# Performance work log

Hardware: AMD Instinct MI355X
Metric: run time of the kernel (lower is better)

## Reference

```python
import jax, jax.numpy as jnp
import numpy as np

N = 4096
IN_F = 128
OUT_F = 64      # per-head out_features
HEADS = 4
ALPHA = 0.2     # LeakyReLU negative slope
NEG_FILL = -9e15


def setup_inputs() -> dict:
    key = jax.random.key(0)
    k_h, k_adj, k_W, k_a = jax.random.split(key, 4)
    h = jax.random.normal(k_h, (N, IN_F), dtype=jnp.float32)
    adj = jax.random.randint(k_adj, (N, N), 0, 2, dtype=jnp.int32)
    W = jax.random.normal(k_W, (IN_F, OUT_F * HEADS), dtype=jnp.float32) * 0.1
    a = jax.random.normal(k_a, (2 * OUT_F, 1), dtype=jnp.float32) * 0.1
    bias = jnp.zeros((OUT_F * HEADS,), dtype=jnp.float32)
    return {"h": h, "adj": adj, "W": W, "a": a, "bias": bias}


def reference(h, adj, W, a, bias):
    n = h.shape[0]
    Wh = (h @ W).reshape(n, HEADS, OUT_F)            # (N, H, F)
    # e_ij = leakyrelu(a_left . Wh_i + a_right . Wh_j)  (decomposed outer sum;
    # same math as concat([Wh_i, Wh_j]) @ a in the original)
    a_left = a[:OUT_F, 0]                            # (F,)
    a_right = a[OUT_F:, 0]                           # (F,)
    left = jnp.einsum('nhf,f->nh', Wh, a_left)       # (N, H)
    right = jnp.einsum('nhf,f->nh', Wh, a_right)     # (N, H)
    mask = adj > 0                                   # (N, N)
    outs = []
    for head in range(HEADS):                        # small fixed loop over heads
        e = left[:, head, None] + right[None, :, head]          # (N, N)
        e = jnp.where(e >= 0, e, ALPHA * e)                      # LeakyReLU
        e = jnp.where(mask, e, NEG_FILL)
        attn = jax.nn.softmax(e, axis=1)                         # (N, N)
        outs.append(attn @ Wh[:, head, :])                       # (N, F)
    out = jnp.concatenate(outs, axis=1)              # concat=True -> (N, H*F)
    return out + bias
```

## Files before the change

kernel.cpp:

```cpp
#include <hip/hip_runtime.h>
#include <hip/hip_bf16.h>

#define NN 4096
#define IN_F 128
#define OUT_F 64
#define C_TOT 256
#define ALPHA 0.2f
#define LOG2E 1.4426950408889634f

typedef float f32x4 __attribute__((ext_vector_type(4)));
typedef __bf16 bf16x8 __attribute__((ext_vector_type(8)));

__device__ __forceinline__ unsigned fmap(float f) {
    unsigned u = __float_as_uint(f);
    return (u >> 31) ? ~u : (u | 0x80000000u);
}
__device__ __forceinline__ float funmap(unsigned u) {
    return (u >> 31) ? __uint_as_float(u & 0x7FFFFFFFu) : __uint_as_float(~u);
}
__device__ __forceinline__ unsigned short bfbits(float x) {
    union { __bf16 b; unsigned short u; } t;
    t.b = (__bf16)x;
    return t.u;
}
__device__ __forceinline__ void gl16(const void* g, void* l) {
    __builtin_amdgcn_global_load_lds((const __attribute__((address_space(1))) void*)g,
                                     (__attribute__((address_space(3))) void*)l, 16, 0, 0);
}
__device__ __forceinline__ void gl4(const void* g, void* l) {
    __builtin_amdgcn_global_load_lds((const __attribute__((address_space(1))) void*)g,
                                     (__attribute__((address_space(3))) void*)l, 4, 0, 0);
}

__global__ __launch_bounds__(256) void k_mask(
    const int* __restrict__ adj, unsigned* __restrict__ mask2,
    const float* __restrict__ W, const float* __restrict__ a,
    unsigned short* __restrict__ WTbf, float* __restrict__ uLR,
    unsigned int* __restrict__ Rmax)
{
    const int tid = threadIdx.x;
    const int lane = tid & 63, wv = tid >> 6;
    const int row = blockIdx.x * 4 + wv;
    const int* __restrict__ ar = adj + (size_t)row * NN;
    const int rg = row >> 6, r64 = row & 63;
    for (int c = 0; c < 8; ++c) {
        const int j0 = c * 512;
        unsigned w = 0u;
#pragma unroll
        for (int k = 0; k < 8; ++k) {
            const unsigned long long bb = __ballot(ar[j0 + k * 64 + lane] > 0);
            const unsigned lo = (unsigned)bb, hi = (unsigned)(bb >> 32);
            if ((lane >> 1) == k) w = (lane & 1) ? hi : lo;
        }
        if (lane < 16) {
            const int wi = c * 16 + lane;
            const int jq = wi >> 5, t = (wi >> 2) & 7, j4 = wi & 3;
            mask2[(size_t)(((rg * 4 + jq) * 8) + t) * 256 + r64 * 4 + j4] = w;
        }
    }

    if (blockIdx.x < 32) {
        const int b = blockIdx.x;
        const int c = b * 8 + (tid & 7);
#pragma unroll
        for (int pass = 0; pass < 4; ++pass) {
            const int k = pass * 32 + (tid >> 3);
            WTbf[(size_t)c * IN_F + k] = bfbits(W[k * C_TOT + c]);
        }
        if (b == 0) {
            if (tid < 4) Rmax[tid] = 0u;
            for (int o = tid; o < 1024; o += 256) {
                const int k = o >> 3, j = o & 7;
                const int hd = j & 3, side = j >> 2;
                float s = 0.f;
                for (int f = 0; f < OUT_F; ++f)
                    s = fmaf(W[k * C_TOT + hd * OUT_F + f], a[side * OUT_F + f], s);
                uLR[k * 8 + side * 4 + hd] = s;
            }
        }
    }
}

__global__ __launch_bounds__(256) void k_prep(
    const float* __restrict__ hmat, const unsigned short* __restrict__ WTbf,
    const float* __restrict__ uLR, unsigned short* __restrict__ WhT,
    float* __restrict__ leftT, float2* __restrict__ erPair,
    unsigned int* __restrict__ Rmax)
{
    __shared__ float hs[16][132];
    __shared__ float us[128][8];
    const int tid = threadIdx.x;
    const int rowbase = blockIdx.x * 16;

    ((float4*)us)[tid] = ((const float4*)uLR)[tid];
#pragma unroll
    for (int p = 0; p < 8; ++p) {
        const int idx = p * 256 + tid;
        hs[idx >> 7][idx & 127] = hmat[(size_t)rowbase * IN_F + idx];
    }
    __syncthreads();

    const int lane = tid & 63, wv = tid >> 6;
    const int m16 = lane & 15, kg = lane >> 4;

    if (wv == 0) {
        const int row = lane >> 2, hd = lane & 3;
        float aL = 0.f, aR = 0.f;
#pragma unroll
        for (int k = 0; k < 128; k += 4) {
            const float4 hv = *(const float4*)&hs[row][k];
            aL = fmaf(hv.x, us[k][hd],   fmaf(hv.y, us[k+1][hd],   fmaf(hv.z, us[k+2][hd],   fmaf(hv.w, us[k+3][hd],   aL))));
            aR = fmaf(hv.x, us[k][hd+4], fmaf(hv.y, us[k+1][hd+4], fmaf(hv.z, us[k+2][hd+4], fmaf(hv.w, us[k+3][hd+4], aR))));
        }
        leftT[hd * NN + rowbase + row] = aL;
        const float rp = aR * LOG2E;
        erPair[(size_t)hd * NN + rowbase + row] = make_float2(exp2f(rp), exp2f(ALPHA * rp));
        float mx = aR;
#pragma unroll
        for (int s = 4; s < 64; s <<= 1) mx = fmaxf(mx, __shfl_xor(mx, s, 64));
        if (lane < 4) atomicMax(&Rmax[hd], fmap(mx));
    }

    bf16x8 afr[4];
#pragma unroll
    for (int ks = 0; ks < 4; ++ks) {
        const float4 lo = *(const float4*)&hs[m16][ks * 32 + kg * 8];
        const float4 hi = *(const float4*)&hs[m16][ks * 32 + kg * 8 + 4];
        bf16x8 v;
        v[0] = (__bf16)lo.x; v[1] = (__bf16)lo.y; v[2] = (__bf16)lo.z; v[3] = (__bf16)lo.w;
        v[4] = (__bf16)hi.x; v[5] = (__bf16)hi.y; v[6] = (__bf16)hi.z; v[7] = (__bf16)hi.w;
        afr[ks] = v;
    }

#pragma unroll
    for (int nt0 = 0; nt0 < 4; ++nt0) {
        const int col = (wv * 4 + nt0) * 16 + m16;
        f32x4 acc = (f32x4){0.f, 0.f, 0.f, 0.f};
#pragma unroll
        for (int ks = 0; ks < 4; ++ks) {
            union { uint4 u; bf16x8 v; } B;
            B.u = *(const uint4*)(WTbf + (size_t)col * IN_F + ks * 32 + kg * 8);
            acc = __builtin_amdgcn_mfma_f32_16x16x32_bf16(afr[ks], B.v, acc, 0, 0, 0);
        }
#pragma unroll
        for (int i = 0; i < 4; ++i)
            WhT[(size_t)col * NN + rowbase + kg * 4 + i] = bfbits(acc[i]);
    }
}

__global__ __launch_bounds__(256, 3) void k_attn(
    const unsigned* __restrict__ mask2,
    const unsigned short* __restrict__ WhT,
    const float* __restrict__ leftT,
    const float2* __restrict__ erPair,
    const unsigned int* __restrict__ Rmax,
    float* __restrict__ out,
    float* __restrict__ num123,
    float* __restrict__ den)
{
    __shared__ unsigned short Bb[2][64 * 128];
    __shared__ float erb[2][256];
    __shared__ unsigned mb[2][256];

    const int tid = threadIdx.x;
    const int lane = tid & 63;
    const int j4 = tid >> 6;
    const int jq = blockIdx.x & 3;
    const int hd = (blockIdx.x >> 2) & 3;
    const int rg = blockIdx.x >> 4;
    const int rowbase = rg * 64;
    const int m = lane & 15;
    const int kg = lane >> 4;
    const int sh = kg * 8;

    const int srow4 = j4 * 4 + (lane >> 4);
    const int g_lin = lane & 15;
    const int lg = g_lin ^ srow4;
    const unsigned short* gB = WhT + (size_t)(hd * 64 + srow4) * NN + jq * 1024 + lg * 8;
    const int dB = srow4 * 128 + g_lin * 8;
    const char* gE = (const char*)(erPair + (size_t)hd * NN + jq * 1024);
    const char* gM = (const char*)mask2 + (size_t)((rg * 4 + jq) * 8) * 1024;
    char* eDst = (char*)&erb[0][0];
    char* mDst = (char*)&mb[0][0];

#define STAGE(buf, t) {                                                        \
    gl16(gB + (t) * 128,                      &Bb[buf][dB]);                   \
    gl16(gB + (t) * 128 + (size_t)16 * NN,    &Bb[buf][dB + 2048]);            \
    gl16(gB + (t) * 128 + (size_t)32 * NN,    &Bb[buf][dB + 4096]);            \
    gl16(gB + (t) * 128 + (size_t)48 * NN,    &Bb[buf][dB + 6144]);            \
    gl4(gE + (t) * 1024 + tid * 4, eDst + (buf) * 1024 + j4 * 256 + lane * 4); \
    gl4(gM + (t) * 1024 + tid * 4, mDst + (buf) * 1024 + j4 * 256 + lane * 4); }

    STAGE(0, 0);

    const float rmx = funmap(Rmax[hd]);
    float EL[4], EL2[4];
#pragma unroll
    for (int rh = 0; rh < 4; ++rh) {
        const float lf = leftT[hd * NN + rowbase + rh * 16 + m];
        const float x = lf + rmx;
        const float mp0 = fmaxf(x, ALPHA * x) * LOG2E;
        EL [rh] = exp2f(fmaf(lf,         LOG2E, -mp0));
        EL2[rh] = exp2f(fmaf(lf * ALPHA, LOG2E, -mp0));
    }
    bf16x8 ONE8;
#pragma unroll
    for (int i = 0; i < 8; ++i) ONE8[i] = (__bf16)1.0f;

    const int pg8 = ((j4 * 4 + kg) ^ m) * 8;
    const int bro = m * 128 + pg8;

    f32x4 acc[4][4], accL[4];
#pragma unroll
    for (int rh = 0; rh < 4; ++rh) {
        accL[rh] = (f32x4){0,0,0,0};
#pragma unroll
        for (int q = 0; q < 4; ++q) acc[rh][q] = (f32x4){0,0,0,0};
    }

    __syncthreads();

#define COMPUTE(buf, t) {                                                      \
    unsigned aw[4];                                                            \
    _Pragma("unroll")                                                          \
    for (int rh = 0; rh < 4; ++rh)                                             \
        aw[rh] = mb[buf][(rh * 16 + m) * 4 + j4] >> sh;                        \
    const char* eb = (const char*)&erb[buf][0] + j4 * 256 + kg * 64;           \
    f32x4 V[4];                                                                \
    _Pragma("unroll")                                                          \
    for (int c = 0; c < 4; ++c) V[c] = *(const f32x4*)(eb + c * 16);           \
    union { __bf16 b[8]; bf16x8 v; } Af[4];                                    \
    _Pragma("unroll")                                                          \
    for (int rh = 0; rh < 4; ++rh) {                                           \
        _Pragma("unroll")                                                      \
        for (int c = 0; c < 4; ++c) {                                          \
            float w0 = fmaxf(V[c].x * EL[rh], V[c].y * EL2[rh]);               \
            float w1 = fmaxf(V[c].z * EL[rh], V[c].w * EL2[rh]);               \
            const unsigned mk0 = (unsigned)(((int)(aw[rh] << (31 - 2*c)))     >> 31); \
            const unsigned mk1 = (unsigned)(((int)(aw[rh] << (31 - (2*c+1)))) >> 31); \
            w0 = __uint_as_float(__float_as_uint(w0) & mk0);                   \
            w1 = __uint_as_float(__float_as_uint(w1) & mk1);                   \
            Af[rh].b[2*c]   = (__bf16)w0;                                      \
            Af[rh].b[2*c+1] = (__bf16)w1;                                      \
        }                                                                      \
    }                                                                          \
    union { uint4 u; bf16x8 v; } B[4];                                         \
    _Pragma("unroll")                                                          \
    for (int q = 0; q < 4; ++q) B[q].u = *(const uint4*)&Bb[buf][bro + q*2048];\
    _Pragma("unroll")                                                          \
    for (int rh = 0; rh < 4; ++rh) {                                           \
        _Pragma("unroll")                                                      \
        for (int q = 0; q < 4; ++q)                                            \
            acc[rh][q] = __builtin_amdgcn_mfma_f32_16x16x32_bf16(Af[rh].v, B[q].v, acc[rh][q], 0, 0, 0); \
        accL[rh] = __builtin_amdgcn_mfma_f32_16x16x32_bf16(Af[rh].v, ONE8, accL[rh], 0, 0, 0); \
    }                                                                          \
}

#pragma unroll
    for (int t = 0; t < 8; ++t) {
        if (t < 7) {
            STAGE((t + 1) & 1, t + 1);
            asm volatile("s_waitcnt vmcnt(6)" ::: "memory");
        } else {
            asm volatile("s_waitcnt vmcnt(0)" ::: "memory");
        }
        __builtin_amdgcn_sched_barrier(0);
        COMPUTE(t & 1, t);
        __builtin_amdgcn_sched_barrier(0);
        __builtin_amdgcn_s_barrier();
    }
#undef STAGE
#undef COMPUTE

    __syncthreads();
    float* comb = (float*)&Bb[0][0];
#pragma unroll
    for (int p = 1; p < 4; ++p) {
        if (j4 == p) {
#pragma unroll
            for (int rh = 0; rh < 4; ++rh) {
#pragma unroll
                for (int q = 0; q < 4; ++q)
                    *(f32x4*)&comb[((rh * 4 + q) * 64 + lane) * 4] = acc[rh][q];
                *(f32x4*)&comb[((16 + rh) * 64 + lane) * 4] = accL[rh];
            }
        }
        __syncthreads();
        if (j4 == 0) {
#pragma unroll
            for (int rh = 0; rh < 4; ++rh) {
#pragma unroll
                for (int q = 0; q < 4; ++q)
                    acc[rh][q] += *(const f32x4*)&comb[((rh * 4 + q) * 64 + lane) * 4];
                accL[rh] += *(const f32x4*)&comb[((16 + rh) * 64 + lane) * 4];
            }
        }
        __syncthreads();
    }

    if (j4 == 0) {
        float* numdst = (jq == 0) ? out : (num123 + (size_t)(jq - 1) * NN * C_TOT);
#pragma unroll
        for (int rh = 0; rh < 4; ++rh) {
#pragma unroll
            for (int q = 0; q < 4; ++q) {
                const int col = hd * 64 + q * 16 + m;
#pragma unroll
                for (int i = 0; i < 4; ++i)
                    numdst[(size_t)(rowbase + rh * 16 + kg * 4 + i) * C_TOT + col] = acc[rh][q][i];
            }
        }
        if (m == 0) {
#pragma unroll
            for (int rh = 0; rh < 4; ++rh)
#pragma unroll
                for (int i = 0; i < 4; ++i)
                    den[(size_t)(jq * 4 + hd) * NN + rowbase + rh * 16 + kg * 4 + i] = accL[rh][i];
        }
    }
}

__global__ __launch_bounds__(256) void k_fin(
    float* __restrict__ out, const float* __restrict__ num123,
    const float* __restrict__ den, const float* __restrict__ bias)
{
    const int idx = blockIdx.x * 256 + threadIdx.x;
    const int row = idx >> 6;
    const int c4 = (idx & 63) * 4;
    const int hd = c4 >> 6;
    const float d = den[(0 * 4 + hd) * NN + row] + den[(1 * 4 + hd) * NN + row]
                  + den[(2 * 4 + hd) * NN + row] + den[(3 * 4 + hd) * NN + row];
    const float rd = 1.0f / d;
    const size_t off = (size_t)row * C_TOT + c4;
    float4 n = *(float4*)(out + off);
    const float4 n1 = *(const float4*)(num123 + off);
    const float4 n2 = *(const float4*)(num123 + (size_t)NN * C_TOT + off);
    const float4 n3 = *(const float4*)(num123 + (size_t)2 * NN * C_TOT + off);
    const float4 bv = *(const float4*)(bias + c4);
    n.x = fmaf(n.x + n1.x + n2.x + n3.x, rd, bv.x);
    n.y = fmaf(n.y + n1.y + n2.y + n3.y, rd, bv.y);
    n.z = fmaf(n.z + n1.z + n2.z + n3.z, rd, bv.z);
    n.w = fmaf(n.w + n1.w + n2.w + n3.w, rd, bv.w);
    *(float4*)(out + off) = n;
}

extern "C" void kernel_launch(void* const* d_in, const int* in_sizes, int n_in,
                              void* d_out, int out_size, void* d_ws, size_t ws_size,
                              hipStream_t stream) {
    const float* hmat = (const float*)d_in[0];
    const int*   adj  = (const int*)d_in[1];
    const float* W    = (const float*)d_in[2];
    const float* a    = (const float*)d_in[3];
    const float* bias = (const float*)d_in[4];
    float* out = (float*)d_out;

    char* ws = (char*)d_ws;
    unsigned short* WhT  = (unsigned short*)(ws + 0x000000);
    float* leftT         = (float*)(ws + 0x2A0000);
    unsigned short* WTbf = (unsigned short*)(ws + 0x2B0000);
    float* uLR           = (float*)(ws + 0x2C0000);
    unsigned int* Rmax   = (unsigned int*)(ws + 0x2C1000);
    float2* erPair       = (float2*)(ws + 0x2C2000);
    unsigned* mask2      = (unsigned*)(ws + 0x300000);
    float* num123        = (float*)(ws + 0x500000);
    float* den           = (float*)(ws + 0x1100000);

    hipLaunchKernelGGL(k_mask, dim3(1024), dim3(256), 0, stream,
                       adj, mask2, W, a, WTbf, uLR, Rmax);
    hipLaunchKernelGGL(k_prep, dim3(256),  dim3(256), 0, stream,
                       hmat, WTbf, uLR, WhT, leftT, erPair, Rmax);
    hipLaunchKernelGGL(k_attn, dim3(1024), dim3(256), 0, stream,
                       mask2, WhT, leftT, erPair, Rmax, out, num123, den);
    hipLaunchKernelGGL(k_fin,  dim3(1024), dim3(256), 0, stream,
                       out, num123, den, bias);
}
```

Measured before the change: 64.85 us.

## Give each attention wave private triple-buffered LDS staging and drop per-tile barriers

The attention kernel stops sharing one double-buffered LDS tile across the block. Each wave now stages its own slice of WhT plus the er/er2 values into a private triple buffer and waits on vmcnt only, so the per-iteration s_barrier goes away. The mask becomes plain row-major and is loaded into registers once up front. The pair exponent array is split into two arrays, and the cross-wave reduction runs in two halves to fit the smaller LDS. The cost is more registers for the mask and a deeper prefetch per wave, which may reduce occupancy.

```diff
diff --git a/kernel.cpp b/kernel.cpp
--- a/kernel.cpp
+++ b/kernel.cpp
@@ -9,6 +9,7 @@
 #define LOG2E 1.4426950408889634f
 
 typedef float f32x4 __attribute__((ext_vector_type(4)));
+typedef float f32x2 __attribute__((ext_vector_type(2)));
 typedef __bf16 bf16x8 __attribute__((ext_vector_type(8)));
 
 __device__ __forceinline__ unsigned fmap(float f) {
@@ -33,7 +34,7 @@
 }
 
 __global__ __launch_bounds__(256) void k_mask(
-    const int* __restrict__ adj, unsigned* __restrict__ mask2,
+    const int* __restrict__ adj, unsigned* __restrict__ mask,
     const float* __restrict__ W, const float* __restrict__ a,
     unsigned short* __restrict__ WTbf, float* __restrict__ uLR,
     unsigned int* __restrict__ Rmax)
@@ -42,7 +43,7 @@
     const int lane = tid & 63, wv = tid >> 6;
     const int row = blockIdx.x * 4 + wv;
     const int* __restrict__ ar = adj + (size_t)row * NN;
-    const int rg = row >> 6, r64 = row & 63;
+    unsigned* __restrict__ mr = mask + (size_t)row * 128;
     for (int c = 0; c < 8; ++c) {
         const int j0 = c * 512;
         unsigned w = 0u;
@@ -52,11 +53,7 @@
             const unsigned lo = (unsigned)bb, hi = (unsigned)(bb >> 32);
             if ((lane >> 1) == k) w = (lane & 1) ? hi : lo;
         }
-        if (lane < 16) {
-            const int wi = c * 16 + lane;
-            const int jq = wi >> 5, t = (wi >> 2) & 7, j4 = wi & 3;
-            mask2[(size_t)(((rg * 4 + jq) * 8) + t) * 256 + r64 * 4 + j4] = w;
-        }
+        if (lane < 16) mr[c * 16 + lane] = w;
     }
 
     if (blockIdx.x < 32) {
@@ -84,7 +81,7 @@
 __global__ __launch_bounds__(256) void k_prep(
     const float* __restrict__ hmat, const unsigned short* __restrict__ WTbf,
     const float* __restrict__ uLR, unsigned short* __restrict__ WhT,
-    float* __restrict__ leftT, float2* __restrict__ erPair,
+    float* __restrict__ leftT, float* __restrict__ er, float* __restrict__ er2,
     unsigned int* __restrict__ Rmax)
 {
     __shared__ float hs[16][132];
@@ -114,7 +111,8 @@
         }
         leftT[hd * NN + rowbase + row] = aL;
         const float rp = aR * LOG2E;
-        erPair[(size_t)hd * NN + rowbase + row] = make_float2(exp2f(rp), exp2f(ALPHA * rp));
+        er [hd * NN + rowbase + row] = exp2f(rp);
+        er2[hd * NN + rowbase + row] = exp2f(ALPHA * rp);
         float mx = aR;
 #pragma unroll
         for (int s = 4; s < 64; s <<= 1) mx = fmaxf(mx, __shfl_xor(mx, s, 64));
@@ -149,173 +147,186 @@
 }
 
 __global__ __launch_bounds__(256, 3) void k_attn(
-    const unsigned* __restrict__ mask2,
+    const unsigned* __restrict__ mask,
     const unsigned short* __restrict__ WhT,
     const float* __restrict__ leftT,
-    const float2* __restrict__ erPair,
+    const float* __restrict__ er,
+    const float* __restrict__ er2,
     const unsigned int* __restrict__ Rmax,
     float* __restrict__ out,
     float* __restrict__ num123,
     float* __restrict__ den)
 {
-    __shared__ unsigned short Bb[2][64 * 128];
-    __shared__ float erb[2][256];
-    __shared__ unsigned mb[2][256];
+    __shared__ char lds[4][3][4352];
 
     const int tid = threadIdx.x;
     const int lane = tid & 63;
-    const int j4 = tid >> 6;
+    const int w = tid >> 6;
     const int jq = blockIdx.x & 3;
     const int hd = (blockIdx.x >> 2) & 3;
-    const int rg = blockIdx.x >> 4;
-    const int rowbase = rg * 64;
+    const int rowbase = (blockIdx.x >> 4) * 64;
     const int m = lane & 15;
     const int kg = lane >> 4;
     const int sh = kg * 8;
-
-    const int srow4 = j4 * 4 + (lane >> 4);
-    const int g_lin = lane & 15;
-    const int lg = g_lin ^ srow4;
-    const unsigned short* gB = WhT + (size_t)(hd * 64 + srow4) * NN + jq * 1024 + lg * 8;
-    const int dB = srow4 * 128 + g_lin * 8;
-    const char* gE = (const char*)(erPair + (size_t)hd * NN + jq * 1024);
-    const char* gM = (const char*)mask2 + (size_t)((rg * 4 + jq) * 8) * 1024;
-    char* eDst = (char*)&erb[0][0];
-    char* mDst = (char*)&mb[0][0];
-
-#define STAGE(buf, t) {                                                        \
-    gl16(gB + (t) * 128,                      &Bb[buf][dB]);                   \
-    gl16(gB + (t) * 128 + (size_t)16 * NN,    &Bb[buf][dB + 2048]);            \
-    gl16(gB + (t) * 128 + (size_t)32 * NN,    &Bb[buf][dB + 4096]);            \
-    gl16(gB + (t) * 128 + (size_t)48 * NN,    &Bb[buf][dB + 6144]);            \
-    gl4(gE + (t) * 1024 + tid * 4, eDst + (buf) * 1024 + j4 * 256 + lane * 4); \
-    gl4(gM + (t) * 1024 + tid * 4, mDst + (buf) * 1024 + j4 * 256 + lane * 4); }
-
-    STAGE(0, 0);
-
+    const int jbase = jq * 1024 + w * 256;
+
+    unsigned mreg[4][8];
+#pragma unroll
+    for (int rb = 0; rb < 4; ++rb) {
+        const unsigned* mrow = mask + (size_t)(rowbase + rb * 16 + m) * 128 + (jbase >> 5);
+        const uint4 v0 = *(const uint4*)(mrow);
+        const uint4 v1 = *(const uint4*)(mrow + 4);
+        mreg[rb][0] = v0.x; mreg[rb][1] = v0.y; mreg[rb][2] = v0.z; mreg[rb][3] = v0.w;
+        mreg[rb][4] = v1.x; mreg[rb][5] = v1.y; mreg[rb][6] = v1.z; mreg[rb][7] = v1.w;
+    }
     const float rmx = funmap(Rmax[hd]);
-    float EL[4], EL2[4];
-#pragma unroll
-    for (int rh = 0; rh < 4; ++rh) {
-        const float lf = leftT[hd * NN + rowbase + rh * 16 + m];
+    f32x2 ELv[4], EL2v[4];
+#pragma unroll
+    for (int rb = 0; rb < 4; ++rb) {
+        const float lf = leftT[hd * NN + rowbase + rb * 16 + m];
         const float x = lf + rmx;
         const float mp0 = fmaxf(x, ALPHA * x) * LOG2E;
-        EL [rh] = exp2f(fmaf(lf,         LOG2E, -mp0));
-        EL2[rh] = exp2f(fmaf(lf * ALPHA, LOG2E, -mp0));
+        const float EL  = exp2f(fmaf(lf,         LOG2E, -mp0));
+        const float EL2 = exp2f(fmaf(lf * ALPHA, LOG2E, -mp0));
+        ELv [rb] = (f32x2){EL,  EL};
+        EL2v[rb] = (f32x2){EL2, EL2};
     }
     bf16x8 ONE8;
 #pragma unroll
     for (int i = 0; i < 8; ++i) ONE8[i] = (__bf16)1.0f;
 
-    const int pg8 = ((j4 * 4 + kg) ^ m) * 8;
-    const int bro = m * 128 + pg8;
+    const unsigned short* bsrc[4];
+#pragma unroll
+    for (int q = 0; q < 4; ++q)
+        bsrc[q] = WhT + (size_t)(hd * 64 + q * 16 + (lane & 15)) * NN
+                  + jbase + (lane >> 4) * 8;
+    const float* esrc = (lane < 32)
+        ? (er  + (size_t)hd * NN + jbase + lane)
+        : (er2 + (size_t)hd * NN + jbase + (lane - 32));
+
+#define STAGE(buf, t) {                                          \
+    char* db = &lds[w][buf][0];                                  \
+    gl16(bsrc[0] + (t) * 32, db +        lane * 16);             \
+    gl16(bsrc[1] + (t) * 32, db + 1024 + lane * 16);             \
+    gl16(bsrc[2] + (t) * 32, db + 2048 + lane * 16);             \
+    gl16(bsrc[3] + (t) * 32, db + 3072 + lane * 16);             \
+    gl4 (esrc    + (t) * 32, db + 4096 + lane * 4);              \
+}
 
     f32x4 acc[4][4], accL[4];
 #pragma unroll
-    for (int rh = 0; rh < 4; ++rh) {
-        accL[rh] = (f32x4){0,0,0,0};
-#pragma unroll
-        for (int q = 0; q < 4; ++q) acc[rh][q] = (f32x4){0,0,0,0};
-    }
-
-    __syncthreads();
-
-#define COMPUTE(buf, t) {                                                      \
-    unsigned aw[4];                                                            \
-    _Pragma("unroll")                                                          \
-    for (int rh = 0; rh < 4; ++rh)                                             \
-        aw[rh] = mb[buf][(rh * 16 + m) * 4 + j4] >> sh;                        \
-    const char* eb = (const char*)&erb[buf][0] + j4 * 256 + kg * 64;           \
-    f32x4 V[4];                                                                \
-    _Pragma("unroll")                                                          \
-    for (int c = 0; c < 4; ++c) V[c] = *(const f32x4*)(eb + c * 16);           \
-    union { __bf16 b[8]; bf16x8 v; } Af[4];                                    \
-    _Pragma("unroll")                                                          \
-    for (int rh = 0; rh < 4; ++rh) {                                           \
-        _Pragma("unroll")                                                      \
-        for (int c = 0; c < 4; ++c) {                                          \
-            float w0 = fmaxf(V[c].x * EL[rh], V[c].y * EL2[rh]);               \
-            float w1 = fmaxf(V[c].z * EL[rh], V[c].w * EL2[rh]);               \
-            const unsigned mk0 = (unsigned)(((int)(aw[rh] << (31 - 2*c)))     >> 31); \
-            const unsigned mk1 = (unsigned)(((int)(aw[rh] << (31 - (2*c+1)))) >> 31); \
-            w0 = __uint_as_float(__float_as_uint(w0) & mk0);                   \
-            w1 = __uint_as_float(__float_as_uint(w1) & mk1);                   \
-            Af[rh].b[2*c]   = (__bf16)w0;                                      \
-            Af[rh].b[2*c+1] = (__bf16)w1;                                      \
-        }                                                                      \
-    }                                                                          \
-    union { uint4 u; bf16x8 v; } B[4];                                         \
-    _Pragma("unroll")                                                          \
-    for (int q = 0; q < 4; ++q) B[q].u = *(const uint4*)&Bb[buf][bro + q*2048];\
-    _Pragma("unroll")                                                          \
-    for (int rh = 0; rh < 4; ++rh) {                                           \
-        _Pragma("unroll")                                                      \
-        for (int q = 0; q < 4; ++q)                                            \
-            acc[rh][q] = __builtin_amdgcn_mfma_f32_16x16x32_bf16(Af[rh].v, B[q].v, acc[rh][q], 0, 0, 0); \
-        accL[rh] = __builtin_amdgcn_mfma_f32_16x16x32_bf16(Af[rh].v, ONE8, accL[rh], 0, 0, 0); \
-    }                                                                          \
-}
-
+    for (int rb = 0; rb < 4; ++rb) {
+        accL[rb] = (f32x4){0,0,0,0};
+#pragma unroll
+        for (int q = 0; q < 4; ++q) acc[rb][q] = (f32x4){0,0,0,0};
+    }
+
+#define COMPUTE(buf, t) {                                                        \
+    const char* wb = &lds[w][buf][0];                                            \
+    const f32x4 E0 = *(const f32x4*)(wb + 4096 + kg * 32);                       \
+    const f32x4 E1 = *(const f32x4*)(wb + 4096 + kg * 32 + 16);                  \
+    const f32x4 F0 = *(const f32x4*)(wb + 4224 + kg * 32);                       \
+    const f32x4 F1 = *(const f32x4*)(wb + 4224 + kg * 32 + 16);                  \
+    union { uint4 u; bf16x8 v; } B0, B1, B2, B3;                                 \
+    B0.u = *(const uint4*)(wb +        lane * 16);                               \
+    B1.u = *(const uint4*)(wb + 1024 + lane * 16);                               \
+    B2.u = *(const uint4*)(wb + 2048 + lane * 16);                               \
+    B3.u = *(const uint4*)(wb + 3072 + lane * 16);                               \
+    const f32x2 ep[4] = { (f32x2){E0.x,E0.y}, (f32x2){E0.z,E0.w},                \
+                          (f32x2){E1.x,E1.y}, (f32x2){E1.z,E1.w} };              \
+    const f32x2 fp[4] = { (f32x2){F0.x,F0.y}, (f32x2){F0.z,F0.w},                \
+                          (f32x2){F1.x,F1.y}, (f32x2){F1.z,F1.w} };              \
+    _Pragma("unroll")                                                            \
+    for (int rb = 0; rb < 4; ++rb) {                                             \
+        const unsigned aw = mreg[rb][(t)] >> sh;                                 \
+        union { __bf16 b[8]; bf16x8 v; } Af;                                     \
+        _Pragma("unroll")                                                        \
+        for (int e = 0; e < 4; ++e) {                                            \
+            const f32x2 full = ep[e] * ELv[rb];                                  \
+            const f32x2 leak = fp[e] * EL2v[rb];                                 \
+            float w0 = fmaxf(full.x, leak.x);                                    \
+            float w1 = fmaxf(full.y, leak.y);                                    \
+            const unsigned mk0 = (unsigned)(((int)(aw << (31 - 2*e)))     >> 31);\
+            const unsigned mk1 = (unsigned)(((int)(aw << (31 - (2*e+1)))) >> 31);\
+            w0 = __uint_as_float(__float_as_uint(w0) & mk0);                     \
+            w1 = __uint_as_float(__float_as_uint(w1) & mk1);                     \
+            Af.b[2*e]   = (__bf16)w0;                                            \
+            Af.b[2*e+1] = (__bf16)w1;                                            \
+        }                                                                        \
+        acc[rb][0] = __builtin_amdgcn_mfma_f32_16x16x32_bf16(Af.v, B0.v, acc[rb][0], 0, 0, 0); \
+        acc[rb][1] = __builtin_amdgcn_mfma_f32_16x16x32_bf16(Af.v, B1.v, acc[rb][1], 0, 0, 0); \
+        acc[rb][2] = __builtin_amdgcn_mfma_f32_16x16x32_bf16(Af.v, B2.v, acc[rb][2], 0, 0, 0); \
+        acc[rb][3] = __builtin_amdgcn_mfma_f32_16x16x32_bf16(Af.v, B3.v, acc[rb][3], 0, 0, 0); \
+        accL[rb]   = __builtin_amdgcn_mfma_f32_16x16x32_bf16(Af.v, ONE8, accL[rb], 0, 0, 0);   \
+    }                                                                            \
+}
+
+    STAGE(0, 0);
+    STAGE(1, 1);
 #pragma unroll
     for (int t = 0; t < 8; ++t) {
-        if (t < 7) {
-            STAGE((t + 1) & 1, t + 1);
-            asm volatile("s_waitcnt vmcnt(6)" ::: "memory");
+        if (t < 6) {
+            STAGE((t + 2) % 3, t + 2);
+            asm volatile("s_waitcnt vmcnt(10)" ::: "memory");
+        } else if (t == 6) {
+            asm volatile("s_waitcnt vmcnt(5)" ::: "memory");
         } else {
             asm volatile("s_waitcnt vmcnt(0)" ::: "memory");
         }
         __builtin_amdgcn_sched_barrier(0);
-        COMPUTE(t & 1, t);
+        COMPUTE(t % 3, t);
         __builtin_amdgcn_sched_barrier(0);
-        __builtin_amdgcn_s_barrier();
     }
 #undef STAGE
 #undef COMPUTE
 
-    __syncthreads();
-    float* comb = (float*)&Bb[0][0];
-#pragma unroll
-    for (int p = 1; p < 4; ++p) {
-        if (j4 == p) {
-#pragma unroll
-            for (int rh = 0; rh < 4; ++rh) {
+    float* comb = (float*)&lds[0][0][0];
+#pragma unroll
+    for (int half = 0; half < 2; ++half) {
+        __syncthreads();
+        if (w > 0) {
+            float* c = comb + ((w - 1) * 64 + lane) * 40;
+#pragma unroll
+            for (int rb2 = 0; rb2 < 2; ++rb2) {
+                const int rb = half * 2 + rb2;
 #pragma unroll
                 for (int q = 0; q < 4; ++q)
-                    *(f32x4*)&comb[((rh * 4 + q) * 64 + lane) * 4] = acc[rh][q];
-                *(f32x4*)&comb[((16 + rh) * 64 + lane) * 4] = accL[rh];
+                    *(f32x4*)&c[rb2 * 20 + q * 4] = acc[rb][q];
+                *(f32x4*)&c[rb2 * 20 + 16] = accL[rb];
             }
         }
         __syncthreads();
-        if (j4 == 0) {
-#pragma unroll
-            for (int rh = 0; rh < 4; ++rh) {
-#pragma unroll
-                for (int q = 0; q < 4; ++q)
-                    acc[rh][q] += *(const f32x4*)&comb[((rh * 4 + q) * 64 + lane) * 4];
-                accL[rh] += *(const f32x4*)&comb[((16 + rh) * 64 + lane) * 4];
+        if (w == 0) {
+#pragma unroll
+            for (int pt = 0; pt < 3; ++pt) {
+                const float* c = comb + (pt * 64 + lane) * 40;
+#pragma unroll
+                for (int rb2 = 0; rb2 < 2; ++rb2) {
+                    const int rb = half * 2 + rb2;
+#pragma unroll
+                    for (int q = 0; q < 4; ++q)
+                        acc[rb][q] += *(const f32x4*)&c[rb2 * 20 + q * 4];
+                    accL[rb] += *(const f32x4*)&c[rb2 * 20 + 16];
+                }
             }
-        }
-        __syncthreads();
-    }
-
-    if (j4 == 0) {
-        float* numdst = (jq == 0) ? out : (num123 + (size_t)(jq - 1) * NN * C_TOT);
-#pragma unroll
-        for (int rh = 0; rh < 4; ++rh) {
-#pragma unroll
-            for (int q = 0; q < 4; ++q) {
-                const int col = hd * 64 + q * 16 + m;
-#pragma unroll
-                for (int i = 0; i < 4; ++i)
-                    numdst[(size_t)(rowbase + rh * 16 + kg * 4 + i) * C_TOT + col] = acc[rh][q][i];
+            float* numdst = (jq == 0) ? out : (num123 + (size_t)(jq - 1) * NN * C_TOT);
+#pragma unroll
+            for (int rb2 = 0; rb2 < 2; ++rb2) {
+                const int rb = half * 2 + rb2;
+                const int rbase = rowbase + rb * 16;
+#pragma unroll
+                for (int q = 0; q < 4; ++q) {
+                    const int col = hd * 64 + q * 16 + m;
+#pragma unroll
+                    for (int i = 0; i < 4; ++i)
+                        numdst[(size_t)(rbase + kg * 4 + i) * C_TOT + col] = acc[rb][q][i];
+                }
+                if (m == 0) {
+#pragma unroll
+                    for (int i = 0; i < 4; ++i)
+                        den[(size_t)(jq * 4 + hd) * NN + rbase + kg * 4 + i] = accL[rb][i];
+                }
             }
-        }
-        if (m == 0) {
-#pragma unroll
-            for (int rh = 0; rh < 4; ++rh)
-#pragma unroll
-                for (int i = 0; i < 4; ++i)
-                    den[(size_t)(jq * 4 + hd) * NN + rowbase + rh * 16 + kg * 4 + i] = accL[rh][i];
         }
     }
 }
@@ -360,17 +371,18 @@
     unsigned short* WTbf = (unsigned short*)(ws + 0x2B0000);
     float* uLR           = (float*)(ws + 0x2C0000);
     unsigned int* Rmax   = (unsigned int*)(ws + 0x2C1000);
-    float2* erPair       = (float2*)(ws + 0x2C2000);
-    unsigned* mask2      = (unsigned*)(ws + 0x300000);
+    float* er            = (float*)(ws + 0x2C2000);
+    float* er2           = (float*)(ws + 0x2D2000);
+    unsigned* mask       = (unsigned*)(ws + 0x300000);
     float* num123        = (float*)(ws + 0x500000);
     float* den           = (float*)(ws + 0x1100000);
 
     hipLaunchKernelGGL(k_mask, dim3(1024), dim3(256), 0, stream,
-                       adj, mask2, W, a, WTbf, uLR, Rmax);
+                       adj, mask, W, a, WTbf, uLR, Rmax);
     hipLaunchKernelGGL(k_prep, dim3(256),  dim3(256), 0, stream,
-                       hmat, WTbf, uLR, WhT, leftT, erPair, Rmax);
+                       hmat, WTbf, uLR, WhT, leftT, er, er2, Rmax);
     hipLaunchKernelGGL(k_attn, dim3(1024), dim3(256), 0, stream,
-                       mask2, WhT, leftT, erPair, Rmax, out, num123, den);
+                       mask, WhT, leftT, er, er2, Rmax, out, num123, den);
     hipLaunchKernelGGL(k_fin,  dim3(1024), dim3(256), 0, stream,
                        out, num123, den, bias);
 }
```

New measurement: 76.28 us. 17.6% more time.
